# Kernel tuning notes

Hardware: AMD Instinct MI355X
Metric: run time of the kernel (lower is better)

The kernel has to match this reference:

```python
import jax, jax.numpy as jnp
import numpy as np

B, T, D, H, C = 64, 2048, 320, 256, 10  # batch, seq, input, hidden, classes


def _lstm_layer(x, W_ih, W_hh, b_ih, b_hh):
    """Single LSTM layer, batch_first x: [B,T,Din] -> [B,T,H].
    PyTorch gate order: i, f, g, o."""
    # Precompute input projections for all timesteps at once (big GEMM, efficient)
    xg = jnp.einsum('btd,gd->btg', x, W_ih) + b_ih + b_hh  # [B,T,4H]
    Hh = W_hh.shape[1]

    def step(carry, xt):
        h, c = carry
        g = xt + h @ W_hh.T  # [B,4H]
        i, f, gg, o = jnp.split(g, 4, axis=-1)
        i = jax.nn.sigmoid(i)
        f = jax.nn.sigmoid(f)
        gg = jnp.tanh(gg)
        o = jax.nn.sigmoid(o)
        c = f * c + i * gg
        h = o * jnp.tanh(c)
        return (h, c), h

    h0 = jnp.zeros((x.shape[0], Hh), x.dtype)
    (_, _), hs = jax.lax.scan(step, (h0, h0), jnp.swapaxes(xg, 0, 1))
    return jnp.swapaxes(hs, 0, 1)  # [B,T,H]


def setup_inputs() -> dict:
    key = jax.random.key(0)
    ks = jax.random.split(key, 12)
    s_ih0 = 1.0 / np.sqrt(H)
    inp = {
        'x': jax.random.normal(ks[0], (B, T, D), dtype=jnp.float32),
        'W_ih0': jax.random.uniform(ks[1], (4 * H, D), jnp.float32, -s_ih0, s_ih0),
        'W_hh0': jax.random.uniform(ks[2], (4 * H, H), jnp.float32, -s_ih0, s_ih0),
        'b_ih0': jax.random.uniform(ks[3], (4 * H,), jnp.float32, -s_ih0, s_ih0),
        'b_hh0': jax.random.uniform(ks[4], (4 * H,), jnp.float32, -s_ih0, s_ih0),
        'W_ih1': jax.random.uniform(ks[5], (4 * H, H), jnp.float32, -s_ih0, s_ih0),
        'W_hh1': jax.random.uniform(ks[6], (4 * H, H), jnp.float32, -s_ih0, s_ih0),
        'b_ih1': jax.random.uniform(ks[7], (4 * H,), jnp.float32, -s_ih0, s_ih0),
        'b_hh1': jax.random.uniform(ks[8], (4 * H,), jnp.float32, -s_ih0, s_ih0),
        'W_fc': jax.random.uniform(ks[9], (C, H), jnp.float32, -s_ih0, s_ih0),
        'b_fc': jax.random.uniform(ks[10], (C,), jnp.float32, -s_ih0, s_ih0),
    }
    return inp


def reference(x, W_ih0, W_hh0, b_ih0, b_hh0, W_ih1, W_hh1, b_ih1, b_hh1, W_fc, b_fc):
    h1 = _lstm_layer(x, W_ih0, W_hh0, b_ih0, b_hh0)   # [B,T,H]
    h2 = _lstm_layer(h1, W_ih1, W_hh1, b_ih1, b_hh1)  # [B,T,H]
    last = h2[:, -1, :]                                # output[:, -1, :]
    return last @ W_fc.T + b_fc                        # [B,C]
```

## Files before the change

### kernel.cpp

```cpp
#include <hip/hip_runtime.h>
#include <stdint.h>

typedef __bf16 bf16x8 __attribute__((ext_vector_type(8)));
typedef float f32x4 __attribute__((ext_vector_type(4)));
typedef unsigned long long u64;

#define BB 64
#define TT 2048
#define DD 320
#define HH 256
#define NC 10
#define GH 1024

#define GB 4
#define GJ 4
#define MB 16
#define JW 64
#define NTHREADS 512
#define SHS 264
#define SGS 260
#define NPAIR 2048
#define NPT 4
#define NRW 3

__device__ __forceinline__ unsigned short f2bf(float f) {
  unsigned u = __float_as_uint(f);
  u += 0x7FFF + ((u >> 16) & 1);
  return (unsigned short)(u >> 16);
}

__global__ void convert_bf16_k(const float* __restrict__ src,
                               unsigned short* __restrict__ dst, int n) {
  int i = blockIdx.x * blockDim.x + threadIdx.x;
  int st = gridDim.x * blockDim.x;
  for (; i < n; i += st) dst[i] = f2bf(src[i]);
}

__global__ void bias_sum_k(const float* __restrict__ a, const float* __restrict__ b,
                           float* __restrict__ d, int n) {
  int i = blockIdx.x * blockDim.x + threadIdx.x;
  if (i < n) d[i] = a[i] + b[i];
}

__device__ __forceinline__ float sigm(float x) { return 1.f / (1.f + __expf(-x)); }
__device__ __forceinline__ float tanh_s(float x) { return 2.f * sigm(2.f * x) - 1.f; }

__device__ __forceinline__ u64 ald(const u64* p) {
  return __hip_atomic_load(p, __ATOMIC_RELAXED, __HIP_MEMORY_SCOPE_AGENT);
}
__device__ __forceinline__ void ast(u64* p, u64 v) {
  __hip_atomic_store(p, v, __ATOMIC_RELAXED, __HIP_MEMORY_SCOPE_AGENT);
}

template <int KCX, bool IS_L0>
__device__ __forceinline__ void lstm_role(
    const unsigned short* __restrict__ xin,
    const u64* __restrict__ xtag,
    const unsigned short* __restrict__ Wih,
    const unsigned short* __restrict__ Whh,
    const float* __restrict__ bias,
    u64* __restrict__ h1out,
    float* __restrict__ hlast,
    u64* __restrict__ hx,
    unsigned short* sX, unsigned short* sH, float* sG,
    int gb, int gj)
{
  constexpr int KX = KCX * 32;
  constexpr int KCH = HH / 32;

  const int tid = threadIdx.x;
  const int wv = tid >> 6;
  const int ln = tid & 63;
  const int lm = ln & 15;
  const int lq = ln >> 4;
  const int j0 = gj * JW;
  const int b0 = gb * MB;

  bf16x8 bW[2][KCX + KCH];
  float bsv[2];
#pragma unroll
  for (int i = 0; i < 2; ++i) {
    int r = (wv * 2 + i) * 16 + lm;
    int grow = (r >> 6) * HH + j0 + (r & 63);
#pragma unroll
    for (int kc = 0; kc < KCX; ++kc)
      bW[i][kc] = *(const bf16x8*)&Wih[(size_t)grow * KX + kc * 32 + lq * 8];
#pragma unroll
    for (int kc = 0; kc < KCH; ++kc)
      bW[i][KCX + kc] = *(const bf16x8*)&Whh[(size_t)grow * HH + kc * 32 + lq * 8];
    bsv[i] = bias[grow];
  }

  int rw[NRW];
#pragma unroll
  for (int i = 0; i < NRW; ++i) {
    int rp = i * NTHREADS + tid;
    int em = rp / 96;
    int q = rp - em * 96;
    int pe = q >> 5;
    pe += (pe >= gj);
    rw[i] = em * 128 + pe * 32 + (q & 31);
  }

  u64* const hxg = hx + (size_t)gb * 2 * NPAIR;
  unsigned* const sHu = (unsigned*)sH;
  unsigned* const sXu = (unsigned*)sX;

  const int emb = tid >> 5;
  const int jp = tid & 31;
  const int jloc = jp * 2;
  const int wpair = emb * 128 + (j0 >> 1) + jp;
  float c0 = 0.f, c1 = 0.f;

  bf16x8 xf[IS_L0 ? KCX : 1];
  u64 qx[NPT];
  if (IS_L0) {
#pragma unroll
    for (int kc = 0; kc < KCX; ++kc)
      xf[kc] = *(const bf16x8*)&xin[((size_t)(b0 + lm) * TT + 0) * KX + kc * 32 + lq * 8];
  } else {
#pragma unroll
    for (int i = 0; i < NPT; ++i) {
      int w = i * NTHREADS + tid;
      qx[i] = ald(&xtag[((size_t)(b0 + (w >> 7)) * TT + 0) * 128 + (w & 127)]);
    }
  }

  __syncthreads();

#pragma unroll 1
  for (int t = 0; t < TT; ++t) {
    u64* const rb = hxg + (size_t)((t + 1) & 1) * NPAIR;
    u64 qh[NRW];
    if (t > 0) {
#pragma unroll
      for (int i = 0; i < NRW; ++i) qh[i] = ald(&rb[rw[i]]);
    }

    f32x4 ac[2][2] = {{{0.f, 0.f, 0.f, 0.f}, {0.f, 0.f, 0.f, 0.f}},
                      {{0.f, 0.f, 0.f, 0.f}, {0.f, 0.f, 0.f, 0.f}}};
    if (IS_L0) {
#pragma unroll
      for (int kc = 0; kc < KCX; ++kc) {
        ac[0][kc & 1] = __builtin_amdgcn_mfma_f32_16x16x32_bf16(xf[kc], bW[0][kc], ac[0][kc & 1], 0, 0, 0);
        ac[1][kc & 1] = __builtin_amdgcn_mfma_f32_16x16x32_bf16(xf[kc], bW[1][kc], ac[1][kc & 1], 0, 0, 0);
      }
    }

    {
      const unsigned etx = (unsigned)(t + 1), eth = (unsigned)t;
      bool ok;
      do {
        bool okx = true, okh = true;
        if (!IS_L0) {
#pragma unroll
          for (int i = 0; i < NPT; ++i) okx &= ((unsigned)(qx[i] >> 32) == etx);
        }
        if (t > 0) {
#pragma unroll
          for (int i = 0; i < NRW; ++i) okh &= ((unsigned)(qh[i] >> 32) == eth);
        }
        ok = okx && okh;
        if (!ok) {
          if (!IS_L0 && !okx) {
#pragma unroll
            for (int i = 0; i < NPT; ++i) {
              int w = i * NTHREADS + tid;
              qx[i] = ald(&xtag[((size_t)(b0 + (w >> 7)) * TT + t) * 128 + (w & 127)]);
            }
          }
          if (t > 0 && !okh) {
#pragma unroll
            for (int i = 0; i < NRW; ++i) qh[i] = ald(&rb[rw[i]]);
          }
        }
      } while (!ok);
    }

    if (!IS_L0) {
#pragma unroll
      for (int i = 0; i < NPT; ++i) {
        int w = i * NTHREADS + tid;
        sXu[(w >> 7) * (SHS / 2) + (w & 127)] = (unsigned)qx[i];
      }
    }
    if (t > 0) {
#pragma unroll
      for (int i = 0; i < NRW; ++i)
        sHu[(rw[i] >> 7) * (SHS / 2) + (rw[i] & 127)] = (unsigned)qh[i];
    }
    __syncthreads();

    if (t + 1 < TT) {
      if (IS_L0) {
#pragma unroll
        for (int kc = 0; kc < KCX; ++kc)
          xf[kc] = *(const bf16x8*)&xin[((size_t)(b0 + lm) * TT + (t + 1)) * KX + kc * 32 + lq * 8];
      } else {
#pragma unroll
        for (int i = 0; i < NPT; ++i) {
          int w = i * NTHREADS + tid;
          qx[i] = ald(&xtag[((size_t)(b0 + (w >> 7)) * TT + (t + 1)) * 128 + (w & 127)]);
        }
      }
    }

    if (!IS_L0) {
#pragma unroll
      for (int kc = 0; kc < KCX; ++kc) {
        bf16x8 a = *(const bf16x8*)&sX[lm * SHS + kc * 32 + lq * 8];
        ac[0][kc & 1] = __builtin_amdgcn_mfma_f32_16x16x32_bf16(a, bW[0][kc], ac[0][kc & 1], 0, 0, 0);
        ac[1][kc & 1] = __builtin_amdgcn_mfma_f32_16x16x32_bf16(a, bW[1][kc], ac[1][kc & 1], 0, 0, 0);
      }
    }
    if (t > 0) {
#pragma unroll
      for (int kc = 0; kc < KCH; ++kc) {
        bf16x8 a = *(const bf16x8*)&sH[lm * SHS + kc * 32 + lq * 8];
        ac[0][kc & 1] = __builtin_amdgcn_mfma_f32_16x16x32_bf16(a, bW[0][KCX + kc], ac[0][kc & 1], 0, 0, 0);
        ac[1][kc & 1] = __builtin_amdgcn_mfma_f32_16x16x32_bf16(a, bW[1][KCX + kc], ac[1][kc & 1], 0, 0, 0);
      }
    }

    f32x4 A0 = ac[0][0] + ac[0][1];
    f32x4 A1 = ac[1][0] + ac[1][1];
#pragma unroll
    for (int r = 0; r < 4; ++r) {
      sG[(lq * 4 + r) * SGS + (wv * 2 + 0) * 16 + lm] = A0[r] + bsv[0];
      sG[(lq * 4 + r) * SGS + (wv * 2 + 1) * 16 + lm] = A1[r] + bsv[1];
    }
    __syncthreads();

    {
      const float* gp = &sG[emb * SGS];
      float gi0 = gp[0 * JW + jloc], gi1 = gp[0 * JW + jloc + 1];
      float gf0 = gp[1 * JW + jloc], gf1 = gp[1 * JW + jloc + 1];
      float gg0 = gp[2 * JW + jloc], gg1 = gp[2 * JW + jloc + 1];
      float go0 = gp[3 * JW + jloc], go1 = gp[3 * JW + jloc + 1];
      c0 = sigm(gf0) * c0 + sigm(gi0) * tanh_s(gg0);
      c1 = sigm(gf1) * c1 + sigm(gi1) * tanh_s(gg1);
      float h0 = sigm(go0) * tanh_s(c0);
      float h1 = sigm(go1) * tanh_s(c1);
      unsigned pair = (unsigned)f2bf(h0) | ((unsigned)f2bf(h1) << 16);
      u64 val = ((u64)(unsigned)(t + 1) << 32) | pair;
      ast(&hxg[(size_t)(t & 1) * NPAIR + wpair], val);
      sHu[emb * (SHS / 2) + (j0 >> 1) + jp] = pair;
      if (IS_L0) {
        ast(&h1out[((size_t)(b0 + emb) * TT + t) * 128 + (j0 >> 1) + jp], val);
      } else if (t == TT - 1) {
        hlast[(size_t)(b0 + emb) * HH + j0 + jloc] = h0;
        hlast[(size_t)(b0 + emb) * HH + j0 + jloc + 1] = h1;
      }
    }
  }
}

__launch_bounds__(NTHREADS, 1)
__global__ void lstm_fused(const unsigned short* __restrict__ xb,
                           u64* __restrict__ h1tag,
                           const unsigned short* __restrict__ Wih0,
                           const unsigned short* __restrict__ Whh0,
                           const float* __restrict__ bias0,
                           const unsigned short* __restrict__ Wih1,
                           const unsigned short* __restrict__ Whh1,
                           const float* __restrict__ bias1,
                           float* __restrict__ h2last,
                           u64* __restrict__ hx0, u64* __restrict__ hx1) {
  __shared__ __align__(16) unsigned short sX[MB * SHS];
  __shared__ __align__(16) unsigned short sH[MB * SHS];
  __shared__ __align__(16) float sG[MB * SGS];
  const int role = blockIdx.x >> 4;
  const int rid = blockIdx.x & 15;
  const int gb = rid >> 2, gj = rid & 3;
  if (role == 0)
    lstm_role<DD / 32, true>(xb, nullptr, Wih0, Whh0, bias0, h1tag, nullptr,
                             hx0, sX, sH, sG, gb, gj);
  else
    lstm_role<HH / 32, false>(nullptr, h1tag, Wih1, Whh1, bias1, nullptr,
                              h2last, hx1, sX, sH, sG, gb, gj);
}

__global__ void fc_k(const float* __restrict__ h, const float* __restrict__ W,
                     const float* __restrict__ b, float* __restrict__ out) {
  int tid = threadIdx.x;
  if (tid < BB * NC) {
    int bb = tid / NC, cc = tid % NC;
    float s = b[cc];
    for (int j = 0; j < HH; ++j) s += h[bb * HH + j] * W[cc * HH + j];
    out[tid] = s;
  }
}

extern "C" void kernel_launch(void* const* d_in, const int* in_sizes, int n_in,
                              void* d_out, int out_size, void* d_ws, size_t ws_size,
                              hipStream_t stream) {
  (void)in_sizes; (void)n_in; (void)out_size;
  const float* x    = (const float*)d_in[0];
  const float* Wih0 = (const float*)d_in[1];
  const float* Whh0 = (const float*)d_in[2];
  const float* bih0 = (const float*)d_in[3];
  const float* bhh0 = (const float*)d_in[4];
  const float* Wih1 = (const float*)d_in[5];
  const float* Whh1 = (const float*)d_in[6];
  const float* bih1 = (const float*)d_in[7];
  const float* bhh1 = (const float*)d_in[8];
  const float* Wfc  = (const float*)d_in[9];
  const float* bfc  = (const float*)d_in[10];

  char* p = (char*)d_ws;
  size_t off = 0;
  auto alloc = [&](size_t bytes) -> char* {
    char* q = p + off;
    off += (bytes + 255) & ~(size_t)255;
    return q;
  };
  u64* hx0 = (u64*)alloc((size_t)GB * 2 * NPAIR * 8);
  u64* hx1 = (u64*)alloc((size_t)GB * 2 * NPAIR * 8);
  float* bias0 = (float*)alloc(GH * 4);
  float* bias1 = (float*)alloc(GH * 4);
  unsigned short* Wih0b = (unsigned short*)alloc((size_t)GH * DD * 2);
  unsigned short* Whh0b = (unsigned short*)alloc((size_t)GH * HH * 2);
  unsigned short* Wih1b = (unsigned short*)alloc((size_t)GH * HH * 2);
  unsigned short* Whh1b = (unsigned short*)alloc((size_t)GH * HH * 2);
  float* h2last = (float*)alloc((size_t)BB * HH * 4);
  unsigned short* xb = (unsigned short*)alloc((size_t)BB * TT * DD * 2);
  u64* h1tag = (u64*)alloc((size_t)BB * TT * (HH / 2) * 8);

  if (ws_size < off) return;

  convert_bf16_k<<<2048, 256, 0, stream>>>(x, xb, BB * TT * DD);
  convert_bf16_k<<<512, 256, 0, stream>>>(Wih0, Wih0b, GH * DD);
  convert_bf16_k<<<512, 256, 0, stream>>>(Whh0, Whh0b, GH * HH);
  convert_bf16_k<<<512, 256, 0, stream>>>(Wih1, Wih1b, GH * HH);
  convert_bf16_k<<<512, 256, 0, stream>>>(Whh1, Whh1b, GH * HH);
  bias_sum_k<<<4, 256, 0, stream>>>(bih0, bhh0, bias0, GH);
  bias_sum_k<<<4, 256, 0, stream>>>(bih1, bhh1, bias1, GH);
  lstm_fused<<<GB * GJ * 2, NTHREADS, 0, stream>>>(
      xb, h1tag, Wih0b, Whh0b, bias0, Wih1b, Whh1b, bias1, h2last, hx0, hx1);
  fc_k<<<1, 640, 0, stream>>>(h2last, Wfc, bfc, (float*)d_out);
}
```

Baseline: 7.158 ms.

## Co-locate each batch group on one XCD and use L2-local sync loads/stores

Launches 64 workgroups and maps blockIdx&7 to the batch group, so the 8 workgroups of each group are expected to share one XCD and its L2. Half of the launched workgroups (gb >= 4) exit immediately. A startup handshake checks that members of each group can see each other's non-coherent stores. If they can, per-timestep h-exchange and layer-0 to layer-1 handoff use plain global loads with sc0 and plain stores instead of agent-scope atomics. This is meant to cut cross-XCD coherence latency on the serial recurrence. It relies on round-robin dispatch placement and falls back to the atomic path if the handshake fails.

```diff
diff --git a/kernel.cpp b/kernel.cpp
--- a/kernel.cpp
+++ b/kernel.cpp
@@ -22,6 +22,9 @@
 #define NPAIR 2048
 #define NPT 4
 #define NRW 3
+#define NWG_LAUNCH 64
+#define HSROUNDS 3
+#define HSSPIN 256
 
 __device__ __forceinline__ unsigned short f2bf(float f) {
   unsigned u = __float_as_uint(f);
@@ -42,6 +45,8 @@
   if (i < n) d[i] = a[i] + b[i];
 }
 
+__global__ void zero_claim_k(int* p) { p[threadIdx.x] = 0; }
+
 __device__ __forceinline__ float sigm(float x) { return 1.f / (1.f + __expf(-x)); }
 __device__ __forceinline__ float tanh_s(float x) { return 2.f * sigm(2.f * x) - 1.f; }
 
@@ -50,6 +55,25 @@
 }
 __device__ __forceinline__ void ast(u64* p, u64 v) {
   __hip_atomic_store(p, v, __ATOMIC_RELAXED, __HIP_MEMORY_SCOPE_AGENT);
+}
+
+__device__ __forceinline__ void st_wt(u64* p, u64 v) {
+  asm volatile("global_store_dwordx2 %0, %1, off" : : "v"(p), "v"(v) : "memory");
+}
+__device__ __forceinline__ void ld_sc0_issue(const u64* p, u64& d) {
+  asm volatile("global_load_dwordx2 %0, %1, off sc0" : "=&v"(d) : "v"(p) : "memory");
+}
+__device__ __forceinline__ u64 ld1_sc0(const u64* p) {
+  u64 v;
+  asm volatile("global_load_dwordx2 %0, %1, off sc0\n\t"
+               "s_waitcnt vmcnt(0)"
+               : "=&v"(v) : "v"(p) : "memory");
+  __builtin_amdgcn_sched_barrier(0);
+  return v;
+}
+__device__ __forceinline__ void vm_wait0() {
+  asm volatile("s_waitcnt vmcnt(0)" ::: "memory");
+  __builtin_amdgcn_sched_barrier(0);
 }
 
 template <int KCX, bool IS_L0>
@@ -63,7 +87,7 @@
     float* __restrict__ hlast,
     u64* __restrict__ hx,
     unsigned short* sX, unsigned short* sH, float* sG,
-    int gb, int gj)
+    int gb, int gj, bool local)
 {
   constexpr int KX = KCX * 32;
   constexpr int KCH = HH / 32;
@@ -122,7 +146,8 @@
 #pragma unroll
     for (int i = 0; i < NPT; ++i) {
       int w = i * NTHREADS + tid;
-      qx[i] = ald(&xtag[((size_t)(b0 + (w >> 7)) * TT + 0) * 128 + (w & 127)]);
+      const u64* p = &xtag[((size_t)(b0 + (w >> 7)) * TT + 0) * 128 + (w & 127)];
+      if (local) ld_sc0_issue(p, qx[i]); else qx[i] = ald(p);
     }
   }
 
@@ -134,7 +159,10 @@
     u64 qh[NRW];
     if (t > 0) {
 #pragma unroll
-      for (int i = 0; i < NRW; ++i) qh[i] = ald(&rb[rw[i]]);
+      for (int i = 0; i < NRW; ++i) {
+        const u64* p = &rb[rw[i]];
+        if (local) ld_sc0_issue(p, qh[i]); else qh[i] = ald(p);
+      }
     }
 
     f32x4 ac[2][2] = {{{0.f, 0.f, 0.f, 0.f}, {0.f, 0.f, 0.f, 0.f}},
@@ -146,6 +174,7 @@
         ac[1][kc & 1] = __builtin_amdgcn_mfma_f32_16x16x32_bf16(xf[kc], bW[1][kc], ac[1][kc & 1], 0, 0, 0);
       }
     }
+    if (local) vm_wait0();
 
     {
       const unsigned etx = (unsigned)(t + 1), eth = (unsigned)t;
@@ -166,13 +195,18 @@
 #pragma unroll
             for (int i = 0; i < NPT; ++i) {
               int w = i * NTHREADS + tid;
-              qx[i] = ald(&xtag[((size_t)(b0 + (w >> 7)) * TT + t) * 128 + (w & 127)]);
+              const u64* p = &xtag[((size_t)(b0 + (w >> 7)) * TT + t) * 128 + (w & 127)];
+              if (local) ld_sc0_issue(p, qx[i]); else qx[i] = ald(p);
             }
           }
           if (t > 0 && !okh) {
 #pragma unroll
-            for (int i = 0; i < NRW; ++i) qh[i] = ald(&rb[rw[i]]);
+            for (int i = 0; i < NRW; ++i) {
+              const u64* p = &rb[rw[i]];
+              if (local) ld_sc0_issue(p, qh[i]); else qh[i] = ald(p);
+            }
           }
+          if (local) vm_wait0();
         }
       } while (!ok);
     }
@@ -200,7 +234,8 @@
 #pragma unroll
         for (int i = 0; i < NPT; ++i) {
           int w = i * NTHREADS + tid;
-          qx[i] = ald(&xtag[((size_t)(b0 + (w >> 7)) * TT + (t + 1)) * 128 + (w & 127)]);
+          const u64* p = &xtag[((size_t)(b0 + (w >> 7)) * TT + (t + 1)) * 128 + (w & 127)];
+          if (local) ld_sc0_issue(p, qx[i]); else qx[i] = ald(p);
         }
       }
     }
@@ -243,10 +278,12 @@
       float h1 = sigm(go1) * tanh_s(c1);
       unsigned pair = (unsigned)f2bf(h0) | ((unsigned)f2bf(h1) << 16);
       u64 val = ((u64)(unsigned)(t + 1) << 32) | pair;
-      ast(&hxg[(size_t)(t & 1) * NPAIR + wpair], val);
+      u64* pw = &hxg[(size_t)(t & 1) * NPAIR + wpair];
+      if (local) st_wt(pw, val); else ast(pw, val);
       sHu[emb * (SHS / 2) + (j0 >> 1) + jp] = pair;
       if (IS_L0) {
-        ast(&h1out[((size_t)(b0 + emb) * TT + t) * 128 + (j0 >> 1) + jp], val);
+        u64* po = &h1out[((size_t)(b0 + emb) * TT + t) * 128 + (j0 >> 1) + jp];
+        if (local) st_wt(po, val); else ast(po, val);
       } else if (t == TT - 1) {
         hlast[(size_t)(b0 + emb) * HH + j0 + jloc] = h0;
         hlast[(size_t)(b0 + emb) * HH + j0 + jloc + 1] = h1;
@@ -265,19 +302,60 @@
                            const unsigned short* __restrict__ Whh1,
                            const float* __restrict__ bias1,
                            float* __restrict__ h2last,
-                           u64* __restrict__ hx0, u64* __restrict__ hx1) {
+                           u64* __restrict__ hx0, u64* __restrict__ hx1,
+                           int* __restrict__ claim) {
   __shared__ __align__(16) unsigned short sX[MB * SHS];
   __shared__ __align__(16) unsigned short sH[MB * SHS];
   __shared__ __align__(16) float sG[MB * SGS];
-  const int role = blockIdx.x >> 4;
-  const int rid = blockIdx.x & 15;
-  const int gb = rid >> 2, gj = rid & 3;
+  __shared__ int sCtl[2];
+
+  const int gb = (int)blockIdx.x & 7;
+  const int sub = (int)blockIdx.x >> 3;
+  if (gb >= GB) return;
+
+  if (threadIdx.x == 0) {
+    u64* hs = (u64*)claim;
+    unsigned* vd = (unsigned*)(claim + 64);
+    const int gid = gb * 8 + sub;
+    bool lok = true;
+    for (int r = 0; r < HSROUNDS && lok; ++r) {
+      st_wt(&hs[gid], ((u64)(0xC0DE0000u + (unsigned)r) << 32) | (unsigned)gid);
+      int it = 0;
+      bool all;
+      do {
+        all = true;
+        for (int m = 0; m < 8; ++m) {
+          u64 v = ld1_sc0(&hs[gb * 8 + m]);
+          unsigned hv = (unsigned)(v >> 32) - 0xC0DE0000u;
+          all &= (hv >= (unsigned)r && hv < (unsigned)HSROUNDS);
+        }
+      } while (!all && ++it < HSSPIN);
+      lok &= all;
+    }
+    __hip_atomic_store(&vd[gid], lok ? 2u : 1u, __ATOMIC_RELAXED,
+                       __HIP_MEMORY_SCOPE_AGENT);
+    bool ul = true;
+    for (int m = 0; m < 8; ++m) {
+      unsigned v;
+      do {
+        v = __hip_atomic_load(&vd[gb * 8 + m], __ATOMIC_RELAXED,
+                              __HIP_MEMORY_SCOPE_AGENT);
+      } while (v == 0);
+      ul &= (v == 2);
+    }
+    sCtl[0] = ul ? 1 : 0;
+  }
+  __syncthreads();
+  const bool local = sCtl[0] != 0;
+
+  const int role = sub >> 2;
+  const int gj = sub & 3;
   if (role == 0)
     lstm_role<DD / 32, true>(xb, nullptr, Wih0, Whh0, bias0, h1tag, nullptr,
-                             hx0, sX, sH, sG, gb, gj);
+                             hx0, sX, sH, sG, gb, gj, local);
   else
     lstm_role<HH / 32, false>(nullptr, h1tag, Wih1, Whh1, bias1, nullptr,
-                              h2last, hx1, sX, sH, sG, gb, gj);
+                              h2last, hx1, sX, sH, sG, gb, gj, local);
 }
 
 __global__ void fc_k(const float* __restrict__ h, const float* __restrict__ W,
@@ -325,9 +403,11 @@
   float* h2last = (float*)alloc((size_t)BB * HH * 4);
   unsigned short* xb = (unsigned short*)alloc((size_t)BB * TT * DD * 2);
   u64* h1tag = (u64*)alloc((size_t)BB * TT * (HH / 2) * 8);
+  int* claim = (int*)alloc(1024);
 
   if (ws_size < off) return;
 
+  zero_claim_k<<<1, 256, 0, stream>>>(claim);
   convert_bf16_k<<<2048, 256, 0, stream>>>(x, xb, BB * TT * DD);
   convert_bf16_k<<<512, 256, 0, stream>>>(Wih0, Wih0b, GH * DD);
   convert_bf16_k<<<512, 256, 0, stream>>>(Whh0, Whh0b, GH * HH);
@@ -335,7 +415,7 @@
   convert_bf16_k<<<512, 256, 0, stream>>>(Whh1, Whh1b, GH * HH);
   bias_sum_k<<<4, 256, 0, stream>>>(bih0, bhh0, bias0, GH);
   bias_sum_k<<<4, 256, 0, stream>>>(bih1, bhh1, bias1, GH);
-  lstm_fused<<<GB * GJ * 2, NTHREADS, 0, stream>>>(
-      xb, h1tag, Wih0b, Whh0b, bias0, Wih1b, Whh1b, bias1, h2last, hx0, hx1);
+  lstm_fused<<<NWG_LAUNCH, NTHREADS, 0, stream>>>(
+      xb, h1tag, Wih0b, Whh0b, bias0, Wih1b, Whh1b, bias1, h2last, hx0, hx1, claim);
   fc_k<<<1, 640, 0, stream>>>(h2last, Wfc, bfc, (float*)d_out);
 }
```

New measurement: 7.206 ms. No clear change (+0.7%).
